# Kernel tuning notes

Hardware: AMD Instinct MI355X
Metric: run time of the kernel (lower is better)

The kernel has to match this reference:

```python
import jax, jax.numpy as jnp
import numpy as np

B, W, D = 8, 1024, 1024
HEADS, KDIM, VDIM = 16, 64, 64


def setup_inputs() -> dict:
    key = jax.random.key(0)
    k1, k2, k3, k4 = jax.random.split(key, 4)
    # he_normal-ish scaling for weights
    s = (2.0 / D) ** 0.5
    return {
        "inputs": jax.random.normal(k1, (B, W, D), dtype=jnp.float32),
        "Wq": jax.random.normal(k2, (D, HEADS * KDIM), dtype=jnp.float32) * s,
        "Wk": jax.random.normal(k3, (D, HEADS * KDIM), dtype=jnp.float32) * s,
        "Wv": jax.random.normal(k4, (D, HEADS * VDIM), dtype=jnp.float32) * s,
    }


def reference(inputs, Wq, Wk, Wv):
    # Self-attention: memory = inputs
    bsz, win, _ = inputs.shape
    # DenseHeads: linear projection, reshaped to (B, W, heads, head_units)
    q = (inputs @ Wq).reshape(bsz, win, HEADS, KDIM)
    k = (inputs @ Wk).reshape(bsz, win, HEADS, KDIM)
    v = (inputs @ Wv).reshape(bsz, win, HEADS, VDIM)
    scale = KDIM ** (-0.5)
    # scores[b,q,h,m] = sum_k Q[b,q,h,k] * K[b,m,h,k]
    scores = jnp.einsum("bqhk,bmhk->bqhm", q, k) * scale
    attn = jax.nn.softmax(scores, axis=-1)
    # out[b,q,h,v] = sum_m attn[b,q,h,m] * V[b,m,h,v]
    out = jnp.einsum("bqhm,bmhv->bqhv", attn, v)
    return out
```

## Files before the change

### kernel.cpp

```cpp
#include <hip/hip_runtime.h>
#include <stdint.h>


using bf16x8 = __attribute__((ext_vector_type(8))) __bf16;
using f32x4  = __attribute__((ext_vector_type(4))) float;

union frag_u { uint4 u4; bf16x8 f; };

__device__ inline unsigned short f2bf(float x){
  unsigned int u = __float_as_uint(x);
  u += 0x7fffu + ((u >> 16) & 1u);
  return (unsigned short)(u >> 16);
}

__device__ inline unsigned int pack2bf(float a, float b){
#if __has_builtin(__builtin_amdgcn_cvt_pk_bf16_f32)
  auto r = __builtin_amdgcn_cvt_pk_bf16_f32(a, b);
  unsigned int u; __builtin_memcpy(&u, &r, 4); return u;
#else
  return (unsigned int)f2bf(a) | ((unsigned int)f2bf(b) << 16);
#endif
}

__device__ inline void gl_lds16(const void* g, void* l){
  __builtin_amdgcn_global_load_lds(
      (const __attribute__((address_space(1))) void*)g,
      (__attribute__((address_space(3))) void*)l, 16, 0, 0);
}

__global__ void cast_x(const float* __restrict__ X, unsigned short* __restrict__ Xb){
  int i = (blockIdx.x * 256 + threadIdx.x) * 4;
  float4 v = *(const float4*)(X + i);
  ushort4 o;
  o.x = f2bf(v.x); o.y = f2bf(v.y); o.z = f2bf(v.z); o.w = f2bf(v.w);
  *(ushort4*)(Xb + i) = o;
}

__global__ void cast_wt(const float* __restrict__ Wq, const float* __restrict__ Wk,
                        const float* __restrict__ Wv, unsigned short* __restrict__ Wt){
  __shared__ float tile[64][65];
  int id = blockIdx.x;
  int proj = id >> 8;
  int rem  = id & 255;
  int kt = rem & 15, nt = rem >> 4;
  const float* Wsrc = (proj == 0) ? Wq : ((proj == 1) ? Wk : Wv);
  int k0 = kt * 64, n0 = nt * 64;
  int tx = threadIdx.x & 63, ty = threadIdx.x >> 6;
  for (int i = 0; i < 16; i++){
    int k = i * 4 + ty;
    tile[k][tx] = Wsrc[(k0 + k) * 1024 + n0 + tx];
  }
  __syncthreads();
  for (int i = 0; i < 16; i++){
    int n = i * 4 + ty;
    Wt[(proj * 1024 + n0 + n) * 1024 + k0 + tx] = f2bf(tile[tx][n]);
  }
}

__global__ void gemm_qkv(const unsigned short* __restrict__ Xb,
                         const unsigned short* __restrict__ Wt,
                         unsigned short* __restrict__ QK,
                         unsigned short* __restrict__ Vt){
  __shared__ __align__(16) unsigned short Abuf[128 * 64];
  __shared__ __align__(16) unsigned short Bbuf[128 * 64];
  int bid = blockIdx.x;
  int bx = bid % 24, by = bid / 24;
  int w = threadIdx.x >> 6, lane = threadIdx.x & 63;
  int g = lane >> 4, li = lane & 15;
  int lrow = lane >> 3, lcol = lane & 7;
  int wm = (w >> 1) * 64, wn = (w & 1) * 64;
  f32x4 acc[4][4] = {};

  for (int k0 = 0; k0 < 1024; k0 += 64){
    __syncthreads();
    for (int i = 0; i < 4; i++){
      int idx = w * 4 + i;
      int row = idx * 8 + lrow;
      gl_lds16(Xb + (by * 128 + row) * 1024 + k0 + lcol * 8, Abuf + idx * 512);
      gl_lds16(Wt + (bx * 128 + row) * 1024 + k0 + lcol * 8, Bbuf + idx * 512);
    }
    __syncthreads();
    for (int c = 0; c < 2; c++){
      frag_u a[4], b[4];
      for (int i = 0; i < 4; i++)
        a[i].u4 = *(const uint4*)(Abuf + (wm + i * 16 + li) * 64 + c * 32 + g * 8);
      for (int j = 0; j < 4; j++)
        b[j].u4 = *(const uint4*)(Bbuf + (wn + j * 16 + li) * 64 + c * 32 + g * 8);
      for (int i = 0; i < 4; i++)
        for (int j = 0; j < 4; j++)
          acc[i][j] = __builtin_amdgcn_mfma_f32_16x16x32_bf16(a[i].f, b[j].f, acc[i][j], 0, 0, 0);
    }
  }
  if (bx >= 16){
    for (int i = 0; i < 4; i++){
      int row = by * 128 + wm + i * 16 + g * 4;
      int bb = row >> 10, m = row & 1023;
      for (int j = 0; j < 4; j++){
        int vc = bx * 128 + wn + j * 16 + li - 2048;
        int hh = vc >> 6, dd = vc & 63;
        ushort4 pk;
        pk.x = f2bf(acc[i][j][0]); pk.y = f2bf(acc[i][j][1]);
        pk.z = f2bf(acc[i][j][2]); pk.w = f2bf(acc[i][j][3]);
        *(ushort4*)(Vt + ((size_t)(bb * 16 + hh) * 64 + dd) * 1024 + m) = pk;
      }
    }
  } else {
    float sc = (bx < 8) ? 0.1803368801111f : 1.0f;
    for (int i = 0; i < 4; i++){
      int row = by * 128 + wm + i * 16 + g * 4;
      for (int j = 0; j < 4; j++){
        int col = bx * 128 + wn + j * 16 + li;
        for (int r = 0; r < 4; r++)
          QK[(size_t)(row + r) * 2048 + col] = f2bf(acc[i][j][r] * sc);
      }
    }
  }
}

__global__ __launch_bounds__(256) void attn(const unsigned short* __restrict__ QK,
                                            const unsigned short* __restrict__ Vt,
                                            float* __restrict__ Out){
  __shared__ __align__(16) unsigned short Kbuf[64 * 64];
  __shared__ __align__(16) unsigned short Vbuf[64 * 64];
  __shared__ __align__(16) unsigned short Pbuf[4][32 * 88];
  int id = blockIdx.x;
  int bh = id >> 3, qb = id & 7;
  int b = bh >> 4, h = bh & 15;
  int w = threadIdx.x >> 6, lane = threadIdx.x & 63;
  int g = lane >> 4, li = lane & 15;
  int lrow = lane >> 3, lcol = lane & 7;
  int scol = ((lcol ^ lrow) & 7) * 8;

  frag_u qf[2][2];
  for (int u = 0; u < 2; u++){
    int tok = b * 1024 + qb * 128 + w * 32 + u * 16 + li;
    const unsigned short* qp = QK + (size_t)tok * 2048 + h * 64 + g * 8;
    qf[u][0].u4 = *(const uint4*)(qp);
    qf[u][1].u4 = *(const uint4*)(qp + 32);
  }

  f32x4 o[2][4] = {};
  float psum[2] = {0.f, 0.f};

  const unsigned short* Kg = QK + (size_t)b * 1024 * 2048 + 1024 + h * 64;
  const unsigned short* Vg = Vt + (size_t)bh * 65536;
  unsigned short* pb = &Pbuf[w][0];

  for (int mt = 0; mt < 16; mt++){
    int m0 = mt * 64;
    __syncthreads();
    for (int i = 0; i < 2; i++){
      int idx = w * 2 + i;
      int row = idx * 8 + lrow;
      gl_lds16(Kg + (size_t)(m0 + row) * 2048 + scol, Kbuf + idx * 512);
      gl_lds16(Vg + row * 1024 + m0 + scol, Vbuf + idx * 512);
    }
    __syncthreads();

    f32x4 s[2][4] = {};
    for (int t = 0; t < 4; t++){
      for (int c = 0; c < 2; c++){
        frag_u kf;
        kf.u4 = *(const uint4*)(Kbuf + (t * 16 + li) * 64 + ((((c << 2) + g) ^ (li & 7)) << 3));
        s[0][t] = __builtin_amdgcn_mfma_f32_16x16x32_bf16(kf.f, qf[0][c].f, s[0][t], 0, 0, 0);
        s[1][t] = __builtin_amdgcn_mfma_f32_16x16x32_bf16(kf.f, qf[1][c].f, s[1][t], 0, 0, 0);
      }
    }

    for (int u = 0; u < 2; u++){
      for (int t = 0; t < 4; t++){
        float p0 = __builtin_exp2f(s[u][t][0]);
        float p1 = __builtin_exp2f(s[u][t][1]);
        float p2 = __builtin_exp2f(s[u][t][2]);
        float p3 = __builtin_exp2f(s[u][t][3]);
        psum[u] += (p0 + p1) + (p2 + p3);
        uint2 pk;
        pk.x = pack2bf(p0, p1);
        pk.y = pack2bf(p2, p3);
        *(uint2*)(pb + (u * 16 + li) * 88 + t * 16 + g * 4) = pk;
      }
    }
    asm volatile("s_waitcnt lgkmcnt(0)" ::: "memory");

    frag_u pf[2][2];
    for (int u = 0; u < 2; u++){
      pf[u][0].u4 = *(const uint4*)(pb + (u * 16 + li) * 88 + g * 8);
      pf[u][1].u4 = *(const uint4*)(pb + (u * 16 + li) * 88 + 32 + g * 8);
    }
    for (int t = 0; t < 4; t++){
      for (int c = 0; c < 2; c++){
        frag_u vf;
        vf.u4 = *(const uint4*)(Vbuf + (t * 16 + li) * 64 + ((((c << 2) + g) ^ (li & 7)) << 3));
        o[0][t] = __builtin_amdgcn_mfma_f32_16x16x32_bf16(vf.f, pf[0][c].f, o[0][t], 0, 0, 0);
        o[1][t] = __builtin_amdgcn_mfma_f32_16x16x32_bf16(vf.f, pf[1][c].f, o[1][t], 0, 0, 0);
      }
    }
  }

  for (int u = 0; u < 2; u++){
    psum[u] += __shfl_xor(psum[u], 16);
    psum[u] += __shfl_xor(psum[u], 32);
  }

  for (int u = 0; u < 2; u++){
    float inv = 1.f / psum[u];
    int tok = b * 1024 + qb * 128 + w * 32 + u * 16 + li;
    float* op = Out + (size_t)tok * 1024 + h * 64 + g * 4;
    for (int t = 0; t < 4; t++){
      float4 v4;
      v4.x = o[u][t][0] * inv; v4.y = o[u][t][1] * inv;
      v4.z = o[u][t][2] * inv; v4.w = o[u][t][3] * inv;
      *(float4*)(op + t * 16) = v4;
    }
  }
}

extern "C" void kernel_launch(void* const* d_in, const int* in_sizes, int n_in,
                              void* d_out, int out_size, void* d_ws, size_t ws_size,
                              hipStream_t stream) {
  const float* X  = (const float*)d_in[0];
  const float* Wq = (const float*)d_in[1];
  const float* Wk = (const float*)d_in[2];
  const float* Wv = (const float*)d_in[3];
  float* Out = (float*)d_out;
  char* ws = (char*)d_ws;
  unsigned short* Xb = (unsigned short*)(ws);
  unsigned short* Wt = (unsigned short*)(ws + (size_t)16 * 1024 * 1024);
  unsigned short* QK = (unsigned short*)(ws + (size_t)22 * 1024 * 1024);
  unsigned short* Vt = (unsigned short*)(ws + (size_t)54 * 1024 * 1024);

  cast_x  <<<8192, 256, 0, stream>>>(X, Xb);
  cast_wt <<<768,  256, 0, stream>>>(Wq, Wk, Wv, Wt);
  gemm_qkv<<<1536, 256, 0, stream>>>(Xb, Wt, QK, Vt);
  attn    <<<1024, 256, 0, stream>>>(QK, Vt, Out);
}
```

Baseline: 225.6 us.

## Keep softmax probabilities in registers via fp16 16x16x16 MFMA for PV

The P·V product now uses the fp16 16x16x16 MFMA, whose B-operand layout matches the S accumulator layout. The exponentiated scores can therefore be packed straight into register fragments, and the LDS P buffer round trip and its wait are gone. V is stored as fp16 for this, and a constant bias of -10 seeds the score accumulators so exp2 stays within fp16 range. The block-index mapping is also swapped so that neighbouring blocks handle different heads. The risks are fp16 overflow or underflow for scores far from the bias, and twice as many smaller MFMA issues.

Result: no change. 221.6 us (-1.7%).

```diff
diff --git a/kernel.cpp b/kernel.cpp
--- a/kernel.cpp
+++ b/kernel.cpp
@@ -4,8 +4,11 @@
 
 using bf16x8 = __attribute__((ext_vector_type(8))) __bf16;
 using f32x4  = __attribute__((ext_vector_type(4))) float;
-
-union frag_u { uint4 u4; bf16x8 f; };
+using f16x4  = __attribute__((ext_vector_type(4))) _Float16;
+
+union frag_u  { uint4 u4; bf16x8 f; };
+union vfrag_u { uint2 u2; f16x4 f; };
+union pfrag_u { unsigned int u[2]; f16x4 f; };
 
 __device__ inline unsigned short f2bf(float x){
   unsigned int u = __float_as_uint(x);
@@ -13,13 +16,9 @@
   return (unsigned short)(u >> 16);
 }
 
-__device__ inline unsigned int pack2bf(float a, float b){
-#if __has_builtin(__builtin_amdgcn_cvt_pk_bf16_f32)
-  auto r = __builtin_amdgcn_cvt_pk_bf16_f32(a, b);
+__device__ inline unsigned int pkrtz_u32(float a, float b){
+  auto r = __builtin_amdgcn_cvt_pkrtz(a, b);
   unsigned int u; __builtin_memcpy(&u, &r, 4); return u;
-#else
-  return (unsigned int)f2bf(a) | ((unsigned int)f2bf(b) << 16);
-#endif
 }
 
 __device__ inline void gl_lds16(const void* g, void* l){
@@ -98,10 +97,10 @@
       for (int j = 0; j < 4; j++){
         int vc = bx * 128 + wn + j * 16 + li - 2048;
         int hh = vc >> 6, dd = vc & 63;
-        ushort4 pk;
-        pk.x = f2bf(acc[i][j][0]); pk.y = f2bf(acc[i][j][1]);
-        pk.z = f2bf(acc[i][j][2]); pk.w = f2bf(acc[i][j][3]);
-        *(ushort4*)(Vt + ((size_t)(bb * 16 + hh) * 64 + dd) * 1024 + m) = pk;
+        uint2 cv;
+        cv.x = pkrtz_u32(acc[i][j][0], acc[i][j][1]);
+        cv.y = pkrtz_u32(acc[i][j][2], acc[i][j][3]);
+        *(uint2*)(Vt + ((size_t)(bb * 16 + hh) * 64 + dd) * 1024 + m) = cv;
       }
     }
   } else {
@@ -122,9 +121,8 @@
                                             float* __restrict__ Out){
   __shared__ __align__(16) unsigned short Kbuf[64 * 64];
   __shared__ __align__(16) unsigned short Vbuf[64 * 64];
-  __shared__ __align__(16) unsigned short Pbuf[4][32 * 88];
   int id = blockIdx.x;
-  int bh = id >> 3, qb = id & 7;
+  int bh = id & 127, qb = id >> 7;
   int b = bh >> 4, h = bh & 15;
   int w = threadIdx.x >> 6, lane = threadIdx.x & 63;
   int g = lane >> 4, li = lane & 15;
@@ -141,10 +139,10 @@
 
   f32x4 o[2][4] = {};
   float psum[2] = {0.f, 0.f};
+  const f32x4 bias = {-10.f, -10.f, -10.f, -10.f};
 
   const unsigned short* Kg = QK + (size_t)b * 1024 * 2048 + 1024 + h * 64;
   const unsigned short* Vg = Vt + (size_t)bh * 65536;
-  unsigned short* pb = &Pbuf[w][0];
 
   for (int mt = 0; mt < 16; mt++){
     int m0 = mt * 64;
@@ -157,7 +155,10 @@
     }
     __syncthreads();
 
-    f32x4 s[2][4] = {};
+    f32x4 s[2][4];
+    for (int u = 0; u < 2; u++)
+      for (int t = 0; t < 4; t++)
+        s[u][t] = bias;
     for (int t = 0; t < 4; t++){
       for (int c = 0; c < 2; c++){
         frag_u kf;
@@ -167,6 +168,7 @@
       }
     }
 
+    pfrag_u pf[2][4];
     for (int u = 0; u < 2; u++){
       for (int t = 0; t < 4; t++){
         float p0 = __builtin_exp2f(s[u][t][0]);
@@ -174,25 +176,18 @@
         float p2 = __builtin_exp2f(s[u][t][2]);
         float p3 = __builtin_exp2f(s[u][t][3]);
         psum[u] += (p0 + p1) + (p2 + p3);
-        uint2 pk;
-        pk.x = pack2bf(p0, p1);
-        pk.y = pack2bf(p2, p3);
-        *(uint2*)(pb + (u * 16 + li) * 88 + t * 16 + g * 4) = pk;
-      }
-    }
-    asm volatile("s_waitcnt lgkmcnt(0)" ::: "memory");
-
-    frag_u pf[2][2];
-    for (int u = 0; u < 2; u++){
-      pf[u][0].u4 = *(const uint4*)(pb + (u * 16 + li) * 88 + g * 8);
-      pf[u][1].u4 = *(const uint4*)(pb + (u * 16 + li) * 88 + 32 + g * 8);
-    }
-    for (int t = 0; t < 4; t++){
-      for (int c = 0; c < 2; c++){
-        frag_u vf;
-        vf.u4 = *(const uint4*)(Vbuf + (t * 16 + li) * 64 + ((((c << 2) + g) ^ (li & 7)) << 3));
-        o[0][t] = __builtin_amdgcn_mfma_f32_16x16x32_bf16(vf.f, pf[0][c].f, o[0][t], 0, 0, 0);
-        o[1][t] = __builtin_amdgcn_mfma_f32_16x16x32_bf16(vf.f, pf[1][c].f, o[1][t], 0, 0, 0);
+        pf[u][t].u[0] = pkrtz_u32(p0, p1);
+        pf[u][t].u[1] = pkrtz_u32(p2, p3);
+      }
+    }
+
+    for (int tv = 0; tv < 4; tv++){
+      for (int t = 0; t < 4; t++){
+        int gg = ((t * 2 + (g >> 1)) ^ (li & 7));
+        vfrag_u vf;
+        vf.u2 = *(const uint2*)(Vbuf + (tv * 16 + li) * 64 + gg * 8 + (g & 1) * 4);
+        o[0][tv] = __builtin_amdgcn_mfma_f32_16x16x16f16(vf.f, pf[0][t].f, o[0][tv], 0, 0, 0);
+        o[1][tv] = __builtin_amdgcn_mfma_f32_16x16x16f16(vf.f, pf[1][t].f, o[1][tv], 0, 0, 0);
       }
     }
   }
@@ -206,11 +201,11 @@
     float inv = 1.f / psum[u];
     int tok = b * 1024 + qb * 128 + w * 32 + u * 16 + li;
     float* op = Out + (size_t)tok * 1024 + h * 64 + g * 4;
-    for (int t = 0; t < 4; t++){
+    for (int tv = 0; tv < 4; tv++){
       float4 v4;
-      v4.x = o[u][t][0] * inv; v4.y = o[u][t][1] * inv;
-      v4.z = o[u][t][2] * inv; v4.w = o[u][t][3] * inv;
-      *(float4*)(op + t * 16) = v4;
+      v4.x = o[u][tv][0] * inv; v4.y = o[u][tv][1] * inv;
+      v4.z = o[u][tv][2] * inv; v4.w = o[u][tv][3] * inv;
+      *(float4*)(op + tv * 16) = v4;
     }
   }
 }
```
